# Kernel tuning notes

Hardware: AMD Instinct MI355X
Metric: run time of the kernel (lower is better)

## Reference

```python
import jax, jax.numpy as jnp
import numpy as np

B, N, E, H = 8, 1024, 768, 8
D = E // H  # 96

def setup_inputs() -> dict:
    key = jax.random.key(0)
    ks = jax.random.split(key, 5)
    s = 0.02
    return {
        "x": jax.random.normal(ks[0], (B, N, E), dtype=jnp.float32),
        "Wqkv": jax.random.normal(ks[1], (E, 3 * E), dtype=jnp.float32) * s,
        "bqkv": jax.random.normal(ks[2], (3 * E,), dtype=jnp.float32) * s,
        "Wproj": jax.random.normal(ks[3], (E, E), dtype=jnp.float32) * s,
        "bproj": jax.random.normal(ks[4], (E,), dtype=jnp.float32) * s,
    }

def reference(x, Wqkv, bqkv, Wproj, bproj):
    # qkv: [B,N,3E] -> split as (h d qkv), qkv fastest-varying -> [B,N,H,D,3]
    qkv = (x @ Wqkv + bqkv).reshape(B, N, H, D, 3)
    q = jnp.transpose(qkv[..., 0], (0, 2, 1, 3))  # [B,H,N,D]
    k = jnp.transpose(qkv[..., 1], (0, 2, 1, 3))
    v = jnp.transpose(qkv[..., 2], (0, 2, 1, 3))
    scale = E ** (-0.5)  # note: emb_size, not head_dim (faithful to source)
    scores = jnp.einsum('bhqd,bhkd->bhqk', q, k) * scale
    attn = jax.nn.softmax(scores, axis=-1)
    out = jnp.einsum('bhqk,bhkd->bhqd', attn, v)  # [B,H,N,D]
    out = jnp.transpose(out, (0, 2, 1, 3)).reshape(B, N, E)
    return out @ Wproj + bproj
```

## Files before the change

### kernel.cpp

```cpp
#include <hip/hip_runtime.h>

typedef unsigned short u16;
typedef __attribute__((ext_vector_type(8))) short short8;
typedef __attribute__((ext_vector_type(4))) short short4v;
typedef __attribute__((ext_vector_type(4))) float f32x4;

#define DEV static __device__ __forceinline__

static_assert(sizeof(short8) == 16, "short8 must be 16B");

DEV u16 f2b(float f) {
  union { float f; unsigned u; } a; a.f = f;
  unsigned u = a.u;
  unsigned r = (u + 0x7FFFu + ((u >> 16) & 1u)) >> 16;
  return (u16)r;
}

DEV f32x4 mfma16(short8 a, short8 b, f32x4 c) {
  asm volatile("v_mfma_f32_16x16x32_bf16 %0, %1, %2, %0" : "+v"(c) : "v"(a), "v"(b));
  return c;
}
DEV f32x4 fence_nops(f32x4 c) { asm volatile("s_nop 7\n\ts_nop 7" : "+v"(c)); return c; }
DEV f32x4 fence0(f32x4 c)     { asm volatile("" : "+v"(c)); return c; }

DEV void gl_lds16(const u16* g, u16* l) {
  __builtin_amdgcn_global_load_lds(
      (const __attribute__((address_space(1))) void*)g,
      (__attribute__((address_space(3))) void*)l, 16, 0, 0);
}

constexpr int Bz = 8, Nseq = 1024, Emb = 768, Hh = 8, Dh = 96;
constexpr int Mrows = Bz * Nseq;
constexpr int K3 = 3 * Emb;
constexpr float QSCALE = 0.05205982021128899f;

__global__ __launch_bounds__(256) void k_cvt_x(const float* __restrict__ src,
                                               u16* __restrict__ dst) {
  int i = (blockIdx.x * 256 + threadIdx.x) * 4;
  float4 v = *(const float4*)(src + i);
  short4v o;
  o[0] = (short)f2b(v.x); o[1] = (short)f2b(v.y);
  o[2] = (short)f2b(v.z); o[3] = (short)f2b(v.w);
  *(short4v*)(dst + i) = o;
}

template <int PERM>
__global__ __launch_bounds__(256) void k_tcvt(const float* __restrict__ src,
                                              u16* __restrict__ dst, int R, int C) {
  __shared__ float t[32][33];
  int bx = blockIdx.x * 32;
  int by = blockIdx.y * 32;
  int c = threadIdx.x & 31, r8 = threadIdx.x >> 5;
#pragma unroll
  for (int p = 0; p < 4; ++p) {
    int r = r8 + p * 8;
    t[r][c] = src[(size_t)(by + r) * C + bx + c];
  }
  __syncthreads();
#pragma unroll
  for (int p = 0; p < 4; ++p) {
    int r = r8 + p * 8;
    int co = bx + r;
    int row = co;
    float mul = 1.f;
    if (PERM) {
      int h = co / 288, rem = co - h * 288;
      int d = rem / 3, s = rem - d * 3;
      row = s * 768 + h * 96 + d;
      if (s == 0) mul = QSCALE;
    }
    dst[(size_t)row * R + by + c] = f2b(t[c][r] * mul);
  }
}

__global__ __launch_bounds__(256) void k_permbias(const float* __restrict__ b,
                                                  float* __restrict__ bp) {
  int co = blockIdx.x * 256 + threadIdx.x;
  if (co < 2304) {
    int h = co / 288, rem = co - h * 288, d = rem / 3, s = rem - d * 3;
    bp[s * 768 + h * 96 + d] = b[co] * (s == 0 ? QSCALE : 1.f);
  }
}

template <int MODE>
__global__ __launch_bounds__(256, 2) void k_gemm_bt(
    const u16* __restrict__ A, const u16* __restrict__ Bt,
    const float* __restrict__ bias,
    u16* __restrict__ obf, u16* __restrict__ vtb, float* __restrict__ of32,
    int Nn, int Kdim) {
  __shared__ __align__(16) u16 Al[128 * 32];
  __shared__ __align__(16) u16 Bl[128 * 32];
  __shared__ __align__(16) u16 Cst[4][32 * 88];
  int m0 = blockIdx.x * 128, n0 = blockIdx.y * 128;
  int tid = threadIdx.x;
  int w = tid >> 6, l = tid & 63, lr = l >> 4, lc = l & 15;
  int wr = w >> 1, wc = w & 1;
  f32x4 acc[4][4] = {};
  int nkt = Kdim >> 5;
  for (int kt = 0; kt < nkt; ++kt) {
    __syncthreads();
#pragma unroll
    for (int i = 0; i < 2; ++i) {
      int idx = i * 256 + tid;
      int r = idx >> 2, c8 = (idx & 3) * 8;
      gl_lds16(A + (size_t)(m0 + r) * Kdim + kt * 32 + c8, &Al[idx * 8]);
      gl_lds16(Bt + (size_t)(n0 + r) * Kdim + kt * 32 + c8, &Bl[idx * 8]);
    }
    __syncthreads();
    short8 af[4];
#pragma unroll
    for (int mi = 0; mi < 4; ++mi)
      af[mi] = *(const short8*)&Al[(wr * 64 + mi * 16 + lc) * 32 + lr * 8];
#pragma unroll
    for (int ni = 0; ni < 4; ++ni) {
      short8 bf = *(const short8*)&Bl[(wc * 64 + ni * 16 + lc) * 32 + lr * 8];
#pragma unroll
      for (int mi = 0; mi < 4; ++mi)
        acc[mi][ni] = mfma16(af[mi], bf, acc[mi][ni]);
    }
  }
  acc[3][3] = fence_nops(acc[3][3]);
#pragma unroll
  for (int mi = 0; mi < 4; ++mi)
#pragma unroll
    for (int ni = 0; ni < 4; ++ni)
      if (!(mi == 3 && ni == 3)) acc[mi][ni] = fence0(acc[mi][ni]);

  if (MODE == 0) {
    if (n0 < 1536) {
      u16* Cb = &Cst[w][0];
#pragma unroll
      for (int mi2 = 0; mi2 < 2; ++mi2) {
#pragma unroll
        for (int mh = 0; mh < 2; ++mh) {
          int mi = mi2 * 2 + mh;
#pragma unroll
          for (int ni = 0; ni < 4; ++ni) {
            float bv = bias[n0 + wc * 64 + ni * 16 + lc];
#pragma unroll
            for (int r = 0; r < 4; ++r)
              Cb[(mh * 16 + lr * 4 + r) * 88 + ni * 16 + lc] =
                  f2b(acc[mi][ni][r] + bv);
          }
        }
#pragma unroll
        for (int i = 0; i < 4; ++i) {
          int idx = i * 64 + l;
          int row = idx >> 3, c8 = idx & 7;
          short8 vv = *(const short8*)&Cb[row * 88 + c8 * 8];
          int grow = m0 + wr * 64 + mi2 * 32 + row;
          int gcol = n0 + wc * 64 + c8 * 8;
          *(short8*)(obf + (size_t)grow * Nn + gcol) = vv;
        }
      }
    } else {
#pragma unroll
      for (int mi = 0; mi < 4; ++mi) {
#pragma unroll
        for (int ni = 0; ni < 4; ++ni) {
          int col = n0 + wc * 64 + ni * 16 + lc;
          float bv = bias[col];
          int dall = col - 1536;
          int row0 = m0 + wr * 64 + mi * 16 + lr * 4;
          short4v o4;
#pragma unroll
          for (int r = 0; r < 4; ++r) o4[r] = (short)f2b(acc[mi][ni][r] + bv);
          *(short4v*)(vtb + ((size_t)(row0 >> 10) * 768 + dall) * 1024 +
                      (row0 & 1023)) = o4;
        }
      }
    }
  } else {
#pragma unroll
    for (int mi = 0; mi < 4; ++mi) {
#pragma unroll
      for (int ni = 0; ni < 4; ++ni) {
        int col = n0 + wc * 64 + ni * 16 + lc;
        float bv = bias[col];
        int row0 = m0 + wr * 64 + mi * 16 + lr * 4;
#pragma unroll
        for (int r = 0; r < 4; ++r)
          of32[(size_t)(row0 + r) * Nn + col] = acc[mi][ni][r] + bv;
      }
    }
  }
}

__global__ __launch_bounds__(256, 2) void k_attn(const u16* __restrict__ qkvp,
                                                 const u16* __restrict__ vt,
                                                 u16* __restrict__ ctx) {
  __shared__ __align__(16) u16 Kb[2][128 * 96];
  __shared__ __align__(16) u16 Pl[4][32 * 40];
  int blk = blockIdx.x;
  int b = blk & 7, h = (blk >> 3) & 7, qt = blk >> 6;
  int tid = threadIdx.x, w = tid >> 6, l = tid & 63;
  int lr = l >> 4, lc = l & 15;
  int q0 = qt * 128 + w * 32;
  const u16* qptr = qkvp + (size_t)b * 1024 * 2304 + h * 96;
  const u16* kptr = qptr + 768;
  const u16* vtp  = vt + (size_t)(b * 768 + h * 96) * 1024;
  u16* Pw = Pl[w];

  int soff[6], doff[6];
#pragma unroll
  for (int i = 0; i < 6; ++i) {
    int idx = i * 256 + tid;
    soff[i] = (idx / 12) * 2304 + (idx % 12) * 8;
    doff[i] = idx * 8;
  }

  short8 qf[2][3];
#pragma unroll
  for (int mf = 0; mf < 2; ++mf)
#pragma unroll
    for (int kf = 0; kf < 3; ++kf)
      qf[mf][kf] = *(const short8*)(qptr + (size_t)(q0 + mf * 16 + lc) * 2304 +
                                    kf * 32 + lr * 8);

  float mrow[2][4], lrow[2][4];
#pragma unroll
  for (int mf = 0; mf < 2; ++mf)
#pragma unroll
    for (int r = 0; r < 4; ++r) { mrow[mf][r] = -INFINITY; lrow[mf][r] = 0.f; }
  f32x4 oacc[2][6] = {};

#pragma unroll
  for (int i = 0; i < 6; ++i) gl_lds16(kptr + soff[i], &Kb[0][0] + doff[i]);
  __syncthreads();

  for (int kt = 0; kt < 8; ++kt) {
    const u16* Kc = Kb[kt & 1];
    if (kt < 7) {
      const u16* kb = kptr + (size_t)(kt + 1) * 128 * 2304;
      u16* db = Kb[(kt + 1) & 1];
#pragma unroll
      for (int i = 0; i < 6; ++i) gl_lds16(kb + soff[i], db + doff[i]);
    }

    f32x4 sacc[2][8] = {};
    __builtin_amdgcn_s_setprio(1);
#pragma unroll
    for (int nf = 0; nf < 8; ++nf) {
#pragma unroll
      for (int kf = 0; kf < 3; ++kf) {
        short8 kb = *(const short8*)&Kc[(nf * 16 + lc) * 96 + kf * 32 + lr * 8];
        sacc[0][nf] = mfma16(qf[0][kf], kb, sacc[0][nf]);
        sacc[1][nf] = mfma16(qf[1][kf], kb, sacc[1][nf]);
      }
    }
    __builtin_amdgcn_s_setprio(0);

    short8 vb[2][6];
    const u16* vkt = vtp + kt * 128;
#pragma unroll
    for (int nf = 0; nf < 6; ++nf)
      vb[0][nf] = *(const short8*)(vkt + (size_t)(nf * 16 + lc) * 1024 + lr * 8);

    sacc[1][7] = fence_nops(sacc[1][7]);
#pragma unroll
    for (int mf = 0; mf < 2; ++mf)
#pragma unroll
      for (int nf = 0; nf < 8; ++nf)
        if (!(mf == 1 && nf == 7)) sacc[mf][nf] = fence0(sacc[mf][nf]);

#pragma unroll
    for (int mf = 0; mf < 2; ++mf) {
#pragma unroll
      for (int r = 0; r < 4; ++r) {
        float mx = sacc[mf][0][r];
#pragma unroll
        for (int nf = 1; nf < 8; ++nf) mx = fmaxf(mx, sacc[mf][nf][r]);
#pragma unroll
        for (int d = 1; d < 16; d <<= 1) mx = fmaxf(mx, __shfl_xor(mx, d));
        if (mx > mrow[mf][r] + 8.f) {
          float sc = exp2f(mrow[mf][r] - mx);
          mrow[mf][r] = mx;
          lrow[mf][r] *= sc;
#pragma unroll
          for (int nf = 0; nf < 6; ++nf) oacc[mf][nf][r] *= sc;
        }
        float m = mrow[mf][r], rs = 0.f;
#pragma unroll
        for (int nf = 0; nf < 8; ++nf) {
          float p = exp2f(sacc[mf][nf][r] - m);
          sacc[mf][nf][r] = p;
          rs += p;
        }
#pragma unroll
        for (int d = 1; d < 16; d <<= 1) rs += __shfl_xor(rs, d);
        lrow[mf][r] += rs;
      }
    }

#pragma unroll
    for (int kf = 0; kf < 4; ++kf) {
      int cb = kf & 1;
#pragma unroll
      for (int mf = 0; mf < 2; ++mf)
#pragma unroll
        for (int nn = 0; nn < 2; ++nn)
#pragma unroll
          for (int r = 0; r < 4; ++r)
            Pw[(mf * 16 + lr * 4 + r) * 40 + nn * 16 + lc] =
                f2b(sacc[mf][2 * kf + nn][r]);
      if (kf < 3) {
#pragma unroll
        for (int nf = 0; nf < 6; ++nf)
          vb[cb ^ 1][nf] = *(const short8*)(vkt + (size_t)(nf * 16 + lc) * 1024 +
                                            (kf + 1) * 32 + lr * 8);
      }
      short8 pa0 = *(const short8*)&Pw[lc * 40 + lr * 8];
      short8 pa1 = *(const short8*)&Pw[(16 + lc) * 40 + lr * 8];
      __builtin_amdgcn_s_setprio(1);
#pragma unroll
      for (int nf = 0; nf < 6; ++nf) {
        oacc[0][nf] = mfma16(pa0, vb[cb][nf], oacc[0][nf]);
        oacc[1][nf] = mfma16(pa1, vb[cb][nf], oacc[1][nf]);
      }
      __builtin_amdgcn_s_setprio(0);
    }
    oacc[1][5] = fence_nops(oacc[1][5]);

    __syncthreads();
  }

#pragma unroll
  for (int mf = 0; mf < 2; ++mf)
#pragma unroll
    for (int nf = 0; nf < 6; ++nf) oacc[mf][nf] = fence0(oacc[mf][nf]);

  u16* Cw = &Kb[0][0] + w * (32 * 104);
  float inv[2][4];
#pragma unroll
  for (int mf = 0; mf < 2; ++mf)
#pragma unroll
    for (int r = 0; r < 4; ++r) inv[mf][r] = 1.0f / lrow[mf][r];
#pragma unroll
  for (int mf = 0; mf < 2; ++mf)
#pragma unroll
    for (int nf = 0; nf < 6; ++nf)
#pragma unroll
      for (int r = 0; r < 4; ++r)
        Cw[(mf * 16 + lr * 4 + r) * 104 + nf * 16 + lc] =
            f2b(oacc[mf][nf][r] * inv[mf][r]);
  int crow0 = b * 1024 + qt * 128 + w * 32;
#pragma unroll
  for (int i = 0; i < 6; ++i) {
    int idx = i * 64 + l;
    int row = idx / 12, c16 = idx % 12;
    short8 vv = *(const short8*)&Cw[row * 104 + c16 * 8];
    *(short8*)(ctx + (size_t)(crow0 + row) * 768 + h * 96 + c16 * 8) = vv;
  }
}

extern "C" void kernel_launch(void* const* d_in, const int* in_sizes, int n_in,
                              void* d_out, int out_size, void* d_ws, size_t ws_size,
                              hipStream_t stream) {
  const float* x     = (const float*)d_in[0];
  const float* Wqkv  = (const float*)d_in[1];
  const float* bqkv  = (const float*)d_in[2];
  const float* Wproj = (const float*)d_in[3];
  const float* bproj = (const float*)d_in[4];
  float* out = (float*)d_out;

  char* ws = (char*)d_ws;
  u16*   xb     = (u16*)(ws);
  u16*   wqkvT  = (u16*)(ws + 12582912);
  u16*   wprojT = (u16*)(ws + 16121856);
  float* bqkvp  = (float*)(ws + 17301504);
  u16*   qkvp   = (u16*)(ws + 17310720);
  u16*   vtb    = (u16*)(ws + 55059456);
  u16*   ctx    = xb;

  k_cvt_x<<<6144, 256, 0, stream>>>(x, xb);
  k_tcvt<1><<<dim3(K3 / 32, Emb / 32), 256, 0, stream>>>(Wqkv, wqkvT, Emb, K3);
  k_tcvt<0><<<dim3(Emb / 32, Emb / 32), 256, 0, stream>>>(Wproj, wprojT, Emb, Emb);
  k_permbias<<<9, 256, 0, stream>>>(bqkv, bqkvp);
  k_gemm_bt<0><<<dim3(Mrows / 128, K3 / 128), 256, 0, stream>>>(
      xb, wqkvT, bqkvp, qkvp, vtb, nullptr, K3, Emb);
  k_attn<<<512, 256, 0, stream>>>(qkvp, vtb, ctx);
  k_gemm_bt<1><<<dim3(Mrows / 128, Emb / 128), 256, 0, stream>>>(
      ctx, wprojT, bproj, nullptr, nullptr, out, Emb, Emb);
}
```

Baseline: 156.9 us.

## Transpose attention MFMAs, shrink K tile to 64, raise occupancy to 3 blocks

The attention kernel now computes S^T = K·Q^T and O^T = V^T·P^T, so each lane holds one query row's scores. That reduces the softmax max/sum reductions to two cross-lane shuffles, and the rescale decision is made wave-wide with __any. K tiles shrink from 128 to 64 keys, which cuts LDS use (one 21.5K-element buffer), and launch bounds go from 2 to 3 blocks per CU. P and the output are packed to bf16 with v_cvt_pk_bf16_f32 and written as 8-byte stores. The cost is twice as many iterations and barriers, tighter register limits that may cause spills, and explicit lgkmcnt waits.

```diff
diff --git a/kernel.cpp b/kernel.cpp
--- a/kernel.cpp
+++ b/kernel.cpp
@@ -4,6 +4,7 @@
 typedef __attribute__((ext_vector_type(8))) short short8;
 typedef __attribute__((ext_vector_type(4))) short short4v;
 typedef __attribute__((ext_vector_type(4))) float f32x4;
+typedef __attribute__((ext_vector_type(2))) unsigned int uint2v;
 
 #define DEV static __device__ __forceinline__
 
@@ -14,6 +15,12 @@
   unsigned u = a.u;
   unsigned r = (u + 0x7FFFu + ((u >> 16) & 1u)) >> 16;
   return (u16)r;
+}
+
+DEV unsigned cvt_pk_bf16(float lo, float hi) {
+  unsigned r;
+  asm("v_cvt_pk_bf16_f32 %0, %1, %2" : "=v"(r) : "v"(lo), "v"(hi));
+  return r;
 }
 
 DEV f32x4 mfma16(short8 a, short8 b, f32x4 c) {
@@ -186,11 +193,10 @@
   }
 }
 
-__global__ __launch_bounds__(256, 2) void k_attn(const u16* __restrict__ qkvp,
+__global__ __launch_bounds__(256, 3) void k_attn(const u16* __restrict__ qkvp,
                                                  const u16* __restrict__ vt,
                                                  u16* __restrict__ ctx) {
-  __shared__ __align__(16) u16 Kb[2][128 * 96];
-  __shared__ __align__(16) u16 Pl[4][32 * 40];
+  __shared__ __align__(16) u16 smem[21504];
   int blk = blockIdx.x;
   int b = blk & 7, h = (blk >> 3) & 7, qt = blk >> 6;
   int tid = threadIdx.x, w = tid >> 6, l = tid & 63;
@@ -199,11 +205,11 @@
   const u16* qptr = qkvp + (size_t)b * 1024 * 2304 + h * 96;
   const u16* kptr = qptr + 768;
   const u16* vtp  = vt + (size_t)(b * 768 + h * 96) * 1024;
-  u16* Pw = Pl[w];
-
-  int soff[6], doff[6];
-#pragma unroll
-  for (int i = 0; i < 6; ++i) {
+  u16* Pw = smem + 12288 + w * 2304;
+
+  int soff[3], doff[3];
+#pragma unroll
+  for (int i = 0; i < 3; ++i) {
     int idx = i * 256 + tid;
     soff[i] = (idx / 12) * 2304 + (idx % 12) * 8;
     doff[i] = idx * 8;
@@ -211,145 +217,150 @@
 
   short8 qf[2][3];
 #pragma unroll
-  for (int mf = 0; mf < 2; ++mf)
+  for (int qi = 0; qi < 2; ++qi)
 #pragma unroll
     for (int kf = 0; kf < 3; ++kf)
-      qf[mf][kf] = *(const short8*)(qptr + (size_t)(q0 + mf * 16 + lc) * 2304 +
+      qf[qi][kf] = *(const short8*)(qptr + (size_t)(q0 + qi * 16 + lc) * 2304 +
                                     kf * 32 + lr * 8);
 
-  float mrow[2][4], lrow[2][4];
-#pragma unroll
-  for (int mf = 0; mf < 2; ++mf)
-#pragma unroll
-    for (int r = 0; r < 4; ++r) { mrow[mf][r] = -INFINITY; lrow[mf][r] = 0.f; }
+  float mrow[2] = {-INFINITY, -INFINITY}, lrow[2] = {0.f, 0.f};
   f32x4 oacc[2][6] = {};
 
 #pragma unroll
-  for (int i = 0; i < 6; ++i) gl_lds16(kptr + soff[i], &Kb[0][0] + doff[i]);
+  for (int i = 0; i < 3; ++i) gl_lds16(kptr + soff[i], smem + doff[i]);
+  short8 va0[6], va1[6];
+#pragma unroll
+  for (int nf = 0; nf < 6; ++nf)
+    va0[nf] = *(const short8*)(vtp + (size_t)(nf * 16 + lc) * 1024 + lr * 8);
   __syncthreads();
 
-  for (int kt = 0; kt < 8; ++kt) {
-    const u16* Kc = Kb[kt & 1];
-    if (kt < 7) {
-      const u16* kb = kptr + (size_t)(kt + 1) * 128 * 2304;
-      u16* db = Kb[(kt + 1) & 1];
-#pragma unroll
-      for (int i = 0; i < 6; ++i) gl_lds16(kb + soff[i], db + doff[i]);
-    }
-
-    f32x4 sacc[2][8] = {};
+  for (int kt = 0; kt < 16; ++kt) {
+    const u16* Kc = smem + (kt & 1) * 6144;
+    if (kt < 15) {
+      const u16* kg = kptr + (size_t)(kt + 1) * 64 * 2304;
+      u16* db = smem + ((kt + 1) & 1) * 6144;
+#pragma unroll
+      for (int i = 0; i < 3; ++i) gl_lds16(kg + soff[i], db + doff[i]);
+    }
+
+    f32x4 sacc[2][4] = {};
     __builtin_amdgcn_s_setprio(1);
 #pragma unroll
-    for (int nf = 0; nf < 8; ++nf) {
+    for (int kfr = 0; kfr < 4; ++kfr) {
 #pragma unroll
       for (int kf = 0; kf < 3; ++kf) {
-        short8 kb = *(const short8*)&Kc[(nf * 16 + lc) * 96 + kf * 32 + lr * 8];
-        sacc[0][nf] = mfma16(qf[0][kf], kb, sacc[0][nf]);
-        sacc[1][nf] = mfma16(qf[1][kf], kb, sacc[1][nf]);
+        short8 kb = *(const short8*)&Kc[(kfr * 16 + lc) * 96 + kf * 32 + lr * 8];
+        sacc[0][kfr] = mfma16(kb, qf[0][kf], sacc[0][kfr]);
+        sacc[1][kfr] = mfma16(kb, qf[1][kf], sacc[1][kfr]);
       }
     }
     __builtin_amdgcn_s_setprio(0);
-
-    short8 vb[2][6];
-    const u16* vkt = vtp + kt * 128;
+    sacc[1][3] = fence_nops(sacc[1][3]);
+#pragma unroll
+    for (int qi = 0; qi < 2; ++qi)
+#pragma unroll
+      for (int kfr = 0; kfr < 4; ++kfr)
+        if (!(qi == 1 && kfr == 3)) sacc[qi][kfr] = fence0(sacc[qi][kfr]);
+
+#pragma unroll
+    for (int qi = 0; qi < 2; ++qi) {
+      float mx = sacc[qi][0][0];
+#pragma unroll
+      for (int kfr = 0; kfr < 4; ++kfr)
+#pragma unroll
+        for (int r = 0; r < 4; ++r)
+          if (kfr | r) mx = fmaxf(mx, sacc[qi][kfr][r]);
+      mx = fmaxf(mx, __shfl_xor(mx, 16));
+      mx = fmaxf(mx, __shfl_xor(mx, 32));
+      if (__any(mx > mrow[qi] + 8.f)) {
+        float nm = fmaxf(mrow[qi], mx);
+        float sc = exp2f(mrow[qi] - nm);
+        mrow[qi] = nm;
+        lrow[qi] *= sc;
+#pragma unroll
+        for (int nf = 0; nf < 6; ++nf)
+#pragma unroll
+          for (int r = 0; r < 4; ++r) oacc[qi][nf][r] *= sc;
+      }
+      float m = mrow[qi], rs = 0.f;
+#pragma unroll
+      for (int kfr = 0; kfr < 4; ++kfr) {
+        float p0 = exp2f(sacc[qi][kfr][0] - m);
+        float p1 = exp2f(sacc[qi][kfr][1] - m);
+        float p2 = exp2f(sacc[qi][kfr][2] - m);
+        float p3 = exp2f(sacc[qi][kfr][3] - m);
+        rs += (p0 + p1) + (p2 + p3);
+        uint2v pk;
+        pk[0] = cvt_pk_bf16(p0, p1);
+        pk[1] = cvt_pk_bf16(p2, p3);
+        *(uint2v*)&Pw[(qi * 16 + lc) * 72 + kfr * 16 + lr * 4] = pk;
+      }
+      rs += __shfl_xor(rs, 16);
+      rs += __shfl_xor(rs, 32);
+      lrow[qi] += rs;
+      if (qi == 0) {
+#pragma unroll
+        for (int nf = 0; nf < 6; ++nf)
+          va1[nf] = *(const short8*)(vtp + (size_t)(nf * 16 + lc) * 1024 +
+                                     kt * 64 + 32 + lr * 8);
+      }
+    }
+    asm volatile("s_waitcnt lgkmcnt(0)" ::: "memory");
+
+    short8 pb0 = *(const short8*)&Pw[lc * 72 + lr * 8];
+    short8 pb1 = *(const short8*)&Pw[(16 + lc) * 72 + lr * 8];
+    __builtin_amdgcn_s_setprio(1);
+#pragma unroll
+    for (int nf = 0; nf < 6; ++nf) {
+      oacc[0][nf] = mfma16(va0[nf], pb0, oacc[0][nf]);
+      oacc[1][nf] = mfma16(va0[nf], pb1, oacc[1][nf]);
+    }
+    __builtin_amdgcn_s_setprio(0);
+    if (kt < 15) {
+#pragma unroll
+      for (int nf = 0; nf < 6; ++nf)
+        va0[nf] = *(const short8*)(vtp + (size_t)(nf * 16 + lc) * 1024 +
+                                   (kt + 1) * 64 + lr * 8);
+    }
+    pb0 = *(const short8*)&Pw[lc * 72 + 32 + lr * 8];
+    pb1 = *(const short8*)&Pw[(16 + lc) * 72 + 32 + lr * 8];
+    __builtin_amdgcn_s_setprio(1);
+#pragma unroll
+    for (int nf = 0; nf < 6; ++nf) {
+      oacc[0][nf] = mfma16(va1[nf], pb0, oacc[0][nf]);
+      oacc[1][nf] = mfma16(va1[nf], pb1, oacc[1][nf]);
+    }
+    __builtin_amdgcn_s_setprio(0);
+    __syncthreads();
+  }
+
+  oacc[1][5] = fence_nops(oacc[1][5]);
+#pragma unroll
+  for (int qi = 0; qi < 2; ++qi)
 #pragma unroll
     for (int nf = 0; nf < 6; ++nf)
-      vb[0][nf] = *(const short8*)(vkt + (size_t)(nf * 16 + lc) * 1024 + lr * 8);
-
-    sacc[1][7] = fence_nops(sacc[1][7]);
-#pragma unroll
-    for (int mf = 0; mf < 2; ++mf)
-#pragma unroll
-      for (int nf = 0; nf < 8; ++nf)
-        if (!(mf == 1 && nf == 7)) sacc[mf][nf] = fence0(sacc[mf][nf]);
-
-#pragma unroll
-    for (int mf = 0; mf < 2; ++mf) {
-#pragma unroll
-      for (int r = 0; r < 4; ++r) {
-        float mx = sacc[mf][0][r];
-#pragma unroll
-        for (int nf = 1; nf < 8; ++nf) mx = fmaxf(mx, sacc[mf][nf][r]);
-#pragma unroll
-        for (int d = 1; d < 16; d <<= 1) mx = fmaxf(mx, __shfl_xor(mx, d));
-        if (mx > mrow[mf][r] + 8.f) {
-          float sc = exp2f(mrow[mf][r] - mx);
-          mrow[mf][r] = mx;
-          lrow[mf][r] *= sc;
-#pragma unroll
-          for (int nf = 0; nf < 6; ++nf) oacc[mf][nf][r] *= sc;
-        }
-        float m = mrow[mf][r], rs = 0.f;
-#pragma unroll
-        for (int nf = 0; nf < 8; ++nf) {
-          float p = exp2f(sacc[mf][nf][r] - m);
-          sacc[mf][nf][r] = p;
-          rs += p;
-        }
-#pragma unroll
-        for (int d = 1; d < 16; d <<= 1) rs += __shfl_xor(rs, d);
-        lrow[mf][r] += rs;
-      }
-    }
-
-#pragma unroll
-    for (int kf = 0; kf < 4; ++kf) {
-      int cb = kf & 1;
-#pragma unroll
-      for (int mf = 0; mf < 2; ++mf)
-#pragma unroll
-        for (int nn = 0; nn < 2; ++nn)
-#pragma unroll
-          for (int r = 0; r < 4; ++r)
-            Pw[(mf * 16 + lr * 4 + r) * 40 + nn * 16 + lc] =
-                f2b(sacc[mf][2 * kf + nn][r]);
-      if (kf < 3) {
-#pragma unroll
-        for (int nf = 0; nf < 6; ++nf)
-          vb[cb ^ 1][nf] = *(const short8*)(vkt + (size_t)(nf * 16 + lc) * 1024 +
-                                            (kf + 1) * 32 + lr * 8);
-      }
-      short8 pa0 = *(const short8*)&Pw[lc * 40 + lr * 8];
-      short8 pa1 = *(const short8*)&Pw[(16 + lc) * 40 + lr * 8];
-      __builtin_amdgcn_s_setprio(1);
-#pragma unroll
-      for (int nf = 0; nf < 6; ++nf) {
-        oacc[0][nf] = mfma16(pa0, vb[cb][nf], oacc[0][nf]);
-        oacc[1][nf] = mfma16(pa1, vb[cb][nf], oacc[1][nf]);
-      }
-      __builtin_amdgcn_s_setprio(0);
-    }
-    oacc[1][5] = fence_nops(oacc[1][5]);
-
-    __syncthreads();
-  }
-
-#pragma unroll
-  for (int mf = 0; mf < 2; ++mf)
-#pragma unroll
-    for (int nf = 0; nf < 6; ++nf) oacc[mf][nf] = fence0(oacc[mf][nf]);
-
-  u16* Cw = &Kb[0][0] + w * (32 * 104);
-  float inv[2][4];
-#pragma unroll
-  for (int mf = 0; mf < 2; ++mf)
-#pragma unroll
-    for (int r = 0; r < 4; ++r) inv[mf][r] = 1.0f / lrow[mf][r];
-#pragma unroll
-  for (int mf = 0; mf < 2; ++mf)
-#pragma unroll
-    for (int nf = 0; nf < 6; ++nf)
-#pragma unroll
-      for (int r = 0; r < 4; ++r)
-        Cw[(mf * 16 + lr * 4 + r) * 104 + nf * 16 + lc] =
-            f2b(oacc[mf][nf][r] * inv[mf][r]);
+      if (!(qi == 1 && nf == 5)) oacc[qi][nf] = fence0(oacc[qi][nf]);
+
+  u16* Cw = smem + w * 3328;
+  float inv[2] = {1.0f / lrow[0], 1.0f / lrow[1]};
+#pragma unroll
+  for (int qi = 0; qi < 2; ++qi) {
+#pragma unroll
+    for (int nf = 0; nf < 6; ++nf) {
+      uint2v pk;
+      pk[0] = cvt_pk_bf16(oacc[qi][nf][0] * inv[qi], oacc[qi][nf][1] * inv[qi]);
+      pk[1] = cvt_pk_bf16(oacc[qi][nf][2] * inv[qi], oacc[qi][nf][3] * inv[qi]);
+      *(uint2v*)&Cw[(qi * 16 + lc) * 104 + nf * 16 + lr * 4] = pk;
+    }
+  }
+  asm volatile("s_waitcnt lgkmcnt(0)" ::: "memory");
   int crow0 = b * 1024 + qt * 128 + w * 32;
 #pragma unroll
   for (int i = 0; i < 6; ++i) {
     int idx = i * 64 + l;
-    int row = idx / 12, c16 = idx % 12;
-    short8 vv = *(const short8*)&Cw[row * 104 + c16 * 8];
-    *(short8*)(ctx + (size_t)(crow0 + row) * 768 + h * 96 + c16 * 8) = vv;
+    int row = idx / 12, c8 = idx % 12;
+    short8 vv = *(const short8*)&Cw[row * 104 + c8 * 8];
+    *(short8*)(ctx + (size_t)(crow0 + row) * 768 + h * 96 + c8 * 8) = vv;
   }
 }
 
```

Result: slower. 168.0 us (+7.1%).
